# Performance work log

Hardware: AMD Instinct MI355X
Metric: run time of the kernel (lower is better)

The kernel has to match this reference:

```python
import jax, jax.numpy as jnp
import numpy as np

CIN, HID, OUT = 128, 256, 349
NTYPES, ETYPES = 4, 5
N0, N1, N2 = 120000, 40000, 10000
GNODES, GEDGES = 250000, 2000000
E0, E1 = 1500000, 400000


def setup_inputs() -> dict:
    key = jax.random.key(0)
    ks = jax.random.split(key, 24)
    ri = jax.random.randint
    rn = jax.random.normal
    inp = {}
    inp['n_id'] = ri(ks[0], (N0,), 0, GNODES)
    inp['x0'] = rn(ks[1], (100000, CIN), dtype=jnp.float32)
    inp['src0'] = ri(ks[2], (E0,), 0, N0)
    inp['dst0'] = ri(ks[3], (E0,), 0, N1)
    inp['e_id0'] = ri(ks[4], (E0,), 0, GEDGES)
    inp['src1'] = ri(ks[5], (E1,), 0, N1)
    inp['dst1'] = ri(ks[6], (E1,), 0, N2)
    inp['e_id1'] = ri(ks[7], (E1,), 0, GEDGES)
    inp['edge_type'] = ri(ks[8], (GEDGES,), 0, ETYPES)
    inp['node_type'] = ri(ks[9], (GNODES,), 0, NTYPES)
    inp['local_node_idx'] = ri(ks[10], (GNODES,), 0, 50000)
    # learned parameters
    inp['emb1'] = rn(ks[11], (50000, CIN), dtype=jnp.float32)
    inp['emb2'] = rn(ks[12], (50000, CIN), dtype=jnp.float32)
    inp['emb3'] = rn(ks[13], (50000, CIN), dtype=jnp.float32)
    s0 = 1.0 / np.sqrt(CIN)
    s1 = 1.0 / np.sqrt(HID)
    inp['relW0'] = rn(ks[14], (ETYPES, CIN, HID), dtype=jnp.float32) * s0
    inp['rootW0'] = rn(ks[15], (NTYPES, CIN, HID), dtype=jnp.float32) * s0
    inp['rootb0'] = rn(ks[16], (NTYPES, HID), dtype=jnp.float32) * 0.02
    inp['relW1'] = rn(ks[17], (ETYPES, HID, OUT), dtype=jnp.float32) * s1
    inp['rootW1'] = rn(ks[18], (NTYPES, HID, OUT), dtype=jnp.float32) * s1
    inp['rootb1'] = rn(ks[19], (NTYPES, OUT), dtype=jnp.float32) * 0.02
    return inp


def _group_input(tables, node_type, local_node_idx, n_id):
    # RGNN.group_input: per-node-type gather from feature / embedding tables.
    nt = node_type[n_id]            # [N0]
    li = local_node_idx[n_id]       # [N0]
    h = jnp.zeros((n_id.shape[0], CIN), dtype=tables[0].dtype)
    for k, tab in enumerate(tables):
        idx = jnp.minimum(li, tab.shape[0] - 1)
        h = jnp.where((nt == k)[:, None], tab[idx], h)
    return h, nt


def _rgcn_layer(x, nt_src, src, dst, et, relW, rootW, rootb, n_tgt):
    # out = sum_t mean-aggregate(x_j over edges of type t) @ W_t  (linear commutes with mean)
    T = relW.shape[0]
    xj = x[src]                                           # [E, Cin] gather
    seg = dst * T + et                                    # fused (target, edge_type) segment id
    sums = jax.ops.segment_sum(xj, seg, num_segments=n_tgt * T)
    cnts = jax.ops.segment_sum(jnp.ones((src.shape[0],), x.dtype), seg, num_segments=n_tgt * T)
    mean = (sums / jnp.maximum(cnts, 1.0)[:, None]).reshape(n_tgt, T, -1)  # [Nt, T, Cin]
    out = jnp.einsum('ntc,tco->no', mean, relW)           # [Nt, Cout]
    # per-node-type root linear: out[mask] += root_lins[i](x_target[mask])
    x_t = x[:n_tgt]
    nt_t = nt_src[:n_tgt]
    allr = jnp.einsum('nc,tco->tno', x_t, rootW) + rootb[:, None, :]  # [Tn, Nt, Cout]
    root = jnp.take_along_axis(allr, nt_t[None, :, None], axis=0)[0]
    return out + root


def reference(n_id, x0, src0, dst0, e_id0, src1, dst1, e_id1, edge_type, node_type,
              local_node_idx, emb1, emb2, emb3, relW0, rootW0, rootb0, relW1, rootW1, rootb1):
    h, nt = _group_input([x0, emb1, emb2, emb3], node_type, local_node_idx, n_id)
    # layer 0: I -> H
    h = _rgcn_layer(h, nt, src0, dst0, edge_type[e_id0], relW0, rootW0, rootb0, N1)
    h = jax.nn.relu(h)
    nt = nt[:N1]
    # layer 1: H -> O
    h = _rgcn_layer(h, nt, src1, dst1, edge_type[e_id1], relW1, rootW1, rootb1, N2)
    return jax.nn.log_softmax(h, axis=-1)
```

## Files before the change

### kernel.cpp

```cpp
#include <hip/hip_runtime.h>
#include <hip/hip_bf16.h>
#include <cmath>

constexpr int kCIN = 128, kHID = 256, kOUT = 349;
constexpr int kNT = 4, kET = 5;
constexpr int kN0 = 120000, kN1 = 40000, kN2 = 10000;
constexpr int kNSEG0 = kN1 * kET;
constexpr int kNSEG1 = kN2 * kET;
constexpr int kNSEG = kNSEG0 + kNSEG1;

constexpr int kBinSegs = 512;
constexpr int kNBin0 = (kNSEG0 + kBinSegs - 1) / kBinSegs;
constexpr int kNBin1 = (kNSEG1 + kBinSegs - 1) / kBinSegs;
constexpr int kNBin  = kNBin0 + kNBin1;
constexpr int kNBLK  = 512;
constexpr int kSB    = 128;

typedef __bf16 bf16x8 __attribute__((ext_vector_type(8)));
typedef float f32x4 __attribute__((ext_vector_type(4)));
typedef float f32x2v __attribute__((ext_vector_type(2)));
typedef unsigned short ushort8v __attribute__((ext_vector_type(8)));

__device__ __forceinline__ unsigned short f2b(float f) {
    unsigned int b = __float_as_uint(f);
    unsigned int r = (b + 0x7FFFu + ((b >> 16) & 1u)) >> 16;
    return (unsigned short)r;
}
__device__ __forceinline__ float b2f(unsigned short u) {
    return __uint_as_float((unsigned int)u << 16);
}
__device__ __forceinline__ void gl2lds16(const void* g, void* l) {
    __builtin_amdgcn_global_load_lds(
        (const __attribute__((address_space(1))) void*)g,
        (__attribute__((address_space(3))) void*)l, 16, 0, 0);
}

__device__ __forceinline__ unsigned int f2e4m3(float f) {
#if __has_builtin(__builtin_amdgcn_cvt_pk_fp8_f32)
    return (unsigned int)(__builtin_amdgcn_cvt_pk_fp8_f32(f, f, 0, false) & 0xFF);
#else
    unsigned int sb = (__float_as_uint(f) >> 31) << 7;
    float m = fminf(fabsf(f), 448.f);
    unsigned int code;
    if (m < 0.015625f) {
        code = (unsigned int)__float2int_rn(m * 512.f);
    } else {
        unsigned int b = __float_as_uint(m);
        b = b + 0x7FFFF + ((b >> 20) & 1);
        int e8 = (int)(b >> 23) - 120;
        if (e8 > 15) code = 0x7E;
        else code = ((unsigned int)e8 << 3) | ((b >> 20) & 7);
    }
    return sb | code;
#endif
}

__device__ __forceinline__ void e4m3x4_to_f32(unsigned int u, float* o4) {
#if __has_builtin(__builtin_amdgcn_cvt_pk_f32_fp8)
    f32x2v a = __builtin_amdgcn_cvt_pk_f32_fp8(u, false);
    f32x2v b = __builtin_amdgcn_cvt_pk_f32_fp8(u, true);
    o4[0] = a[0]; o4[1] = a[1]; o4[2] = b[0]; o4[3] = b[1];
#else
#pragma unroll
    for (int i = 0; i < 4; i++) {
        unsigned int c = (u >> (8 * i)) & 0xFF;
        unsigned int s = c >> 7, e = (c >> 3) & 15, mm = c & 7;
        float v;
        if (e == 0) v = (float)mm * 0.001953125f;
        else        v = __uint_as_float((e + 120u) << 23 | mm << 20);
        o4[i] = s ? -v : v;
    }
#endif
}

__global__ void k_et8(const int* __restrict__ etype, unsigned char* __restrict__ et8, int n)
{
    int i = blockIdx.x * 256 + threadIdx.x;
    if (i < n) et8[i] = (unsigned char)etype[i];
}

__global__ void k_gather(const int* __restrict__ n_id, const float* __restrict__ x0,
                         const float* __restrict__ e1, const float* __restrict__ e2,
                         const float* __restrict__ e3, const int* __restrict__ ntype,
                         const int* __restrict__ lidx, unsigned short* __restrict__ h0b,
                         unsigned char* __restrict__ h0f8, int* __restrict__ nt0)
{
    int row = blockIdx.x * 8 + (threadIdx.x >> 5);
    if (row >= kN0) return;
    int lane = threadIdx.x & 31;
    int gid = n_id[row];
    int nt = ntype[gid];
    int li = lidx[gid];
    const float* tab;
    int rows;
    if (nt == 0)      { tab = x0; rows = 100000; }
    else if (nt == 1) { tab = e1; rows = 50000; }
    else if (nt == 2) { tab = e2; rows = 50000; }
    else              { tab = e3; rows = 50000; }
    int idx = li < rows ? li : rows - 1;
    float4 v = reinterpret_cast<const float4*>(tab + (size_t)idx * kCIN)[lane];
    ushort4 o;
    o.x = f2b(v.x); o.y = f2b(v.y); o.z = f2b(v.z); o.w = f2b(v.w);
    reinterpret_cast<ushort4*>(h0b + (size_t)row * kCIN)[lane] = o;
    unsigned int q = f2e4m3(v.x) | (f2e4m3(v.y) << 8) | (f2e4m3(v.z) << 16) | (f2e4m3(v.w) << 24);
    reinterpret_cast<unsigned int*>(h0f8 + (size_t)row * kCIN)[lane] = q;
    if (lane == 0) nt0[row] = nt;
}

__global__ __launch_bounds__(1024) void k_bincnt(
    const int* __restrict__ dst0, const int* __restrict__ eid0, int E0,
    const int* __restrict__ dst1, const int* __restrict__ eid1, int E1,
    const unsigned char* __restrict__ et8, int* __restrict__ cnts2d,
    int* __restrict__ seg32,
    const int* __restrict__ nt0, int* __restrict__ ntcnts)
{
    __shared__ int h[kNBin];
    const int tid = threadIdx.x;
    if (blockIdx.x < kNBLK) {
        for (int k = tid; k < kNBin; k += 1024) h[k] = 0;
        __syncthreads();
        int Etot = E0 + E1;
        int chunk = (Etot + kNBLK - 1) / kNBLK;
        int lo = blockIdx.x * chunk;
        int hi = min(lo + chunk, Etot);
        for (int i = lo + tid; i < hi; i += 1024) {
            int c;
            if (i < E0) c = dst0[i] * kET + (int)et8[eid0[i]];
            else { int e = i - E0; c = kNBin0 * kBinSegs + dst1[e] * kET + (int)et8[eid1[e]]; }
            seg32[i] = c;
            atomicAdd(&h[c >> 9], 1);
        }
        __syncthreads();
        for (int k = tid; k < kNBin; k += 1024) cnts2d[(size_t)k * kNBLK + blockIdx.x] = h[k];
    } else {
        int b = blockIdx.x - kNBLK;
        int layer = b >= kSB;
        int blk = b - layer * kSB;
        int M = layer ? kN2 : kN1;
        if (tid < 4) h[tid] = 0;
        __syncthreads();
        int chunk = (M + kSB - 1) / kSB;
        int lo = blk * chunk, hi = min(lo + chunk, M);
        for (int i = lo + tid; i < hi; i += 1024) atomicAdd(&h[nt0[i]], 1);
        __syncthreads();
        if (tid < 4) ntcnts[(layer * 4 + tid) * kSB + blk] = h[tid];
    }
}

__global__ void k_scan1(const int* __restrict__ cnt, int* __restrict__ excl,
                        int* __restrict__ blksum, int n)
{
    __shared__ int sm[1024];
    int i = blockIdx.x * 1024 + threadIdx.x;
    int v = (i < n) ? cnt[i] : 0;
    sm[threadIdx.x] = v;
    __syncthreads();
    for (int off = 1; off < 1024; off <<= 1) {
        int t = (threadIdx.x >= off) ? sm[threadIdx.x - off] : 0;
        __syncthreads();
        sm[threadIdx.x] += t;
        __syncthreads();
    }
    if (i < n) excl[i] = sm[threadIdx.x] - v;
    if (threadIdx.x == 1023) blksum[blockIdx.x] = sm[1023];
}

__global__ __launch_bounds__(1024) void k_scan2(
    int* __restrict__ blksum, int nblk,
    const int* __restrict__ ntcnts, int* __restrict__ ntoffs,
    int* __restrict__ goff0, int* __restrict__ goff1)
{
    __shared__ int sm[1024];
    int tid = threadIdx.x;
    if (blockIdx.x == 0) {
        int v = (tid < nblk) ? blksum[tid] : 0;
        sm[tid] = v;
        __syncthreads();
        for (int off = 1; off < 1024; off <<= 1) {
            int t = (tid >= off) ? sm[tid - off] : 0;
            __syncthreads();
            sm[tid] += t;
            __syncthreads();
        }
        if (tid < nblk) blksum[tid] = sm[tid] - v;
    } else {
        int v = ntcnts[tid];
        sm[tid] = v;
        __syncthreads();
        for (int off = 1; off < 512; off <<= 1) {
            int t = 0;
            if ((tid & 511) >= off) t = sm[tid - off];
            __syncthreads();
            sm[tid] += t;
            __syncthreads();
        }
        int excl = sm[tid] - v;
        ntoffs[tid] = excl;
        if ((tid & 127) == 0) {
            int layer = tid >> 9;
            int t = (tid >> 7) & 3;
            if (layer == 0) goff0[t] = excl; else goff1[t] = excl;
        }
        if (tid == 0) { goff0[4] = kN1; goff1[4] = kN2; }
    }
}

__global__ __launch_bounds__(1024) void k_binplace(
    const int* __restrict__ src0, int E0,
    const int* __restrict__ src1, int E1,
    const int* __restrict__ seg32,
    const int* __restrict__ offs2d, const int* __restrict__ blksum,
    unsigned int* __restrict__ pairs,
    const int* __restrict__ nt0, const int* __restrict__ ntoffs,
    int* __restrict__ perm0, int* __restrict__ perm1)
{
    __shared__ int cur[kNBin];
    const int tid = threadIdx.x;
    if (blockIdx.x < kNBLK) {
        for (int k = tid; k < kNBin; k += 1024) {
            size_t li = (size_t)k * kNBLK + blockIdx.x;
            cur[k] = offs2d[li] + blksum[li >> 10];
        }
        __syncthreads();
        int Etot = E0 + E1;
        int chunk = (Etot + kNBLK - 1) / kNBLK;
        int lo = blockIdx.x * chunk;
        int hi = min(lo + chunk, Etot);
        for (int i = lo + tid; i < hi; i += 1024) {
            int c = seg32[i];
            int s = (i < E0) ? src0[i] : src1[i - E0];
            unsigned int pay = (unsigned int)s | ((unsigned int)(c & (kBinSegs - 1)) << 17);
            int p = atomicAdd(&cur[c >> 9], 1);
            pairs[p] = pay;
        }
    } else {
        int b = blockIdx.x - kNBLK;
        int layer = b >= kSB;
        int blk = b - layer * kSB;
        int M = layer ? kN2 : kN1;
        int* perm = layer ? perm1 : perm0;
        if (tid < 4) cur[tid] = ntoffs[(layer * 4 + tid) * kSB + blk];
        __syncthreads();
        int chunk = (M + kSB - 1) / kSB;
        int lo = blk * chunk, hi = min(lo + chunk, M);
        for (int i = lo + tid; i < hi; i += 1024) {
            int p = atomicAdd(&cur[nt0[i]], 1);
            perm[p] = i;
        }
    }
}

__global__ __launch_bounds__(1024) void k_binscatter(
    const int* __restrict__ offs2d, const int* __restrict__ blksum, int Etot,
    const unsigned int* __restrict__ pairs,
    int* __restrict__ order, int* __restrict__ starts, int* __restrict__ cnt)
{
    __shared__ int h[kBinSegs];
    __shared__ int sc[kBinSegs];
    __shared__ int cur[kBinSegs];
    const int bin = blockIdx.x;
    const int tid = threadIdx.x;
    size_t bi = (size_t)bin * kNBLK;
    const int base = offs2d[bi] + blksum[bi >> 10];
    int end = Etot;
    if (bin + 1 < kNBin) {
        size_t ei = (size_t)(bin + 1) * kNBLK;
        end = offs2d[ei] + blksum[ei >> 10];
    }
    const int c = end - base;
    const unsigned int* pp = pairs + base;

    for (int k = tid; k < kBinSegs; k += 1024) h[k] = 0;
    __syncthreads();
    for (int j = tid; j < c; j += 1024) atomicAdd(&h[pp[j] >> 17], 1);
    __syncthreads();
    if (tid < kBinSegs) sc[tid] = h[tid];
    __syncthreads();
    for (int off = 1; off < kBinSegs; off <<= 1) {
        int t = 0;
        if (tid < kBinSegs && tid >= off) t = sc[tid - off];
        __syncthreads();
        if (tid < kBinSegs) sc[tid] += t;
        __syncthreads();
    }
    int seg_rel, abs_base, seglim;
    if (bin < kNBin0) { seg_rel = bin * kBinSegs; abs_base = seg_rel; seglim = kNSEG0 - seg_rel; }
    else { seg_rel = (bin - kNBin0) * kBinSegs; abs_base = kNSEG0 + seg_rel; seglim = kNSEG1 - seg_rel; }
    if (tid < kBinSegs) {
        int excl = sc[tid] - h[tid];
        cur[tid] = excl;
        if (tid < seglim) {
            starts[abs_base + tid] = base + excl;
            cnt[abs_base + tid] = h[tid];
        }
    }
    __syncthreads();
    for (int j = tid; j < c; j += 1024) {
        unsigned int u = pp[j];
        int sl = (int)(u >> 17);
        int p = atomicAdd(&cur[sl], 1);
        order[base + p] = (int)(u & 0x1FFFFu);
    }
}

__global__ __launch_bounds__(256) void k_segreduce8(
    const int* __restrict__ starts, const int* __restrict__ cnt,
    const int* __restrict__ order, const unsigned char* __restrict__ h8,
    unsigned short* __restrict__ mean, int nseg)
{
    constexpr int C = kCIN;
    constexpr int L = C / 8;
    constexpr int SPB = 256 / L;
    int sidx = blockIdx.x * SPB + threadIdx.x / L;
    if (sidx >= nseg) return;
    int lane = threadIdx.x % L;
    int st = starts[sidx];
    int n = cnt[sidx];
    const unsigned char* hp = h8 + (size_t)lane * 8;
    float a[4][8];
#pragma unroll
    for (int u = 0; u < 4; u++)
#pragma unroll
        for (int i = 0; i < 8; i++) a[u][i] = 0.f;
    int j = 0;
    for (; j + 4 <= n; j += 4) {
        int s0 = order[st + j + 0];
        int s1 = order[st + j + 1];
        int s2 = order[st + j + 2];
        int s3 = order[st + j + 3];
        uint2 u0 = *reinterpret_cast<const uint2*>(hp + (size_t)s0 * C);
        uint2 u1 = *reinterpret_cast<const uint2*>(hp + (size_t)s1 * C);
        uint2 u2 = *reinterpret_cast<const uint2*>(hp + (size_t)s2 * C);
        uint2 u3 = *reinterpret_cast<const uint2*>(hp + (size_t)s3 * C);
        float d[8];
        e4m3x4_to_f32(u0.x, d); e4m3x4_to_f32(u0.y, d + 4);
#pragma unroll
        for (int i = 0; i < 8; i++) a[0][i] += d[i];
        e4m3x4_to_f32(u1.x, d); e4m3x4_to_f32(u1.y, d + 4);
#pragma unroll
        for (int i = 0; i < 8; i++) a[1][i] += d[i];
        e4m3x4_to_f32(u2.x, d); e4m3x4_to_f32(u2.y, d + 4);
#pragma unroll
        for (int i = 0; i < 8; i++) a[2][i] += d[i];
        e4m3x4_to_f32(u3.x, d); e4m3x4_to_f32(u3.y, d + 4);
#pragma unroll
        for (int i = 0; i < 8; i++) a[3][i] += d[i];
    }
    for (; j < n; ++j) {
        int s0 = order[st + j];
        uint2 u0 = *reinterpret_cast<const uint2*>(hp + (size_t)s0 * C);
        float d[8];
        e4m3x4_to_f32(u0.x, d); e4m3x4_to_f32(u0.y, d + 4);
#pragma unroll
        for (int i = 0; i < 8; i++) a[0][i] += d[i];
    }
    float sc = 1.0f / fmaxf((float)n, 1.0f);
    ushort8v o;
#pragma unroll
    for (int i = 0; i < 8; i++) o[i] = f2b(((a[0][i] + a[1][i]) + (a[2][i] + a[3][i])) * sc);
    *reinterpret_cast<ushort8v*>(mean + (size_t)sidx * C + lane * 8) = o;
}

template<int C>
__global__ __launch_bounds__(256) void k_segreduce(
    const int* __restrict__ starts, const int* __restrict__ cnt,
    const int* __restrict__ order, const unsigned short* __restrict__ h,
    unsigned short* __restrict__ mean, int nseg)
{
    constexpr int L = C / 8;
    constexpr int SPB = 256 / L;
    int sidx = blockIdx.x * SPB + threadIdx.x / L;
    if (sidx >= nseg) return;
    int lane = threadIdx.x % L;
    int st = starts[sidx];
    int n = cnt[sidx];
    const unsigned short* hp = h + (size_t)lane * 8;
    float a[4][8];
#pragma unroll
    for (int u = 0; u < 4; u++)
#pragma unroll
        for (int i = 0; i < 8; i++) a[u][i] = 0.f;
    int j = 0;
    for (; j + 4 <= n; j += 4) {
        int s0 = order[st + j + 0];
        int s1 = order[st + j + 1];
        int s2 = order[st + j + 2];
        int s3 = order[st + j + 3];
        ushort8v v0 = *reinterpret_cast<const ushort8v*>(hp + (size_t)s0 * C);
        ushort8v v1 = *reinterpret_cast<const ushort8v*>(hp + (size_t)s1 * C);
        ushort8v v2 = *reinterpret_cast<const ushort8v*>(hp + (size_t)s2 * C);
        ushort8v v3 = *reinterpret_cast<const ushort8v*>(hp + (size_t)s3 * C);
#pragma unroll
        for (int i = 0; i < 8; i++) {
            a[0][i] += b2f(v0[i]); a[1][i] += b2f(v1[i]);
            a[2][i] += b2f(v2[i]); a[3][i] += b2f(v3[i]);
        }
    }
    for (; j < n; ++j) {
        int s0 = order[st + j];
        ushort8v v0 = *reinterpret_cast<const ushort8v*>(hp + (size_t)s0 * C);
#pragma unroll
        for (int i = 0; i < 8; i++) a[0][i] += b2f(v0[i]);
    }
    float sc = 1.0f / fmaxf((float)n, 1.0f);
    ushort8v o;
#pragma unroll
    for (int i = 0; i < 8; i++) o[i] = f2b(((a[0][i] + a[1][i]) + (a[2][i] + a[3][i])) * sc);
    *reinterpret_cast<ushort8v*>(mean + (size_t)sidx * C + lane * 8) = o;
}

__global__ void k_prepw2(const float* __restrict__ relW0, const float* __restrict__ rootW0,
                         unsigned short* __restrict__ Bt0T,
                         const float* __restrict__ relW1, const float* __restrict__ rootW1,
                         unsigned short* __restrict__ Bt1T)
{
    constexpr int T0 = kNT * 256 * 768;
    constexpr int T1 = kNT * 384 * 1536;
    int i = blockIdx.x * 256 + threadIdx.x;
    if (i < T0) {
        int g = i / (256 * 768);
        int rem = i - g * (256 * 768);
        int col = rem / 768;
        int k = rem - col * 768;
        float v = (k < 640) ? relW0[(size_t)k * 256 + col]
                            : rootW0[((size_t)g * 128 + (k - 640)) * 256 + col];
        Bt0T[i] = f2b(v);
    } else if (i < T0 + T1) {
        int ii = i - T0;
        int g = ii / (384 * 1536);
        int rem = ii - g * (384 * 1536);
        int col = rem / 1536;
        int k = rem - col * 1536;
        float v = 0.f;
        if (col < kOUT) v = (k < 1280) ? relW1[(size_t)k * kOUT + col]
                                       : rootW1[((size_t)g * 256 + (k - 1280)) * kOUT + col];
        Bt1T[ii] = f2b(v);
    }
}

template<int C, int BM, int BN, int RELU, int OUTBF16>
__global__ __launch_bounds__(256) void k_gemm_sorted(
    int M, int Nreal, int NpadK,
    const unsigned short* __restrict__ meanb,
    const unsigned short* __restrict__ hb,
    const unsigned short* __restrict__ BtT,
    const float* __restrict__ rootb,
    const int* __restrict__ perm, const int* __restrict__ goff,
    unsigned short* __restrict__ outb, float* __restrict__ outf)
{
    constexpr int K1 = kET * C;
    constexpr int K  = K1 + C;
    constexpr int FM = BM / 32;
    constexpr int FN = BN / 32;
    __shared__ __align__(16) char ldsA[BM * 128];
    __shared__ __align__(16) char ldsB[BN * 128];

    int g, row0s = 0, gend = 0;
    {
        int gs0 = goff[0], gs1 = goff[1], gs2 = goff[2], gs3 = goff[3], gs4 = goff[4];
        int gs[5] = {gs0, gs1, gs2, gs3, gs4};
        int t = blockIdx.x, tb = 0;
        for (g = 0; g < 4; ++g) {
            int cg = gs[g + 1] - gs[g];
            int ntl = (cg + BM - 1) / BM;
            if (t < tb + ntl) { row0s = gs[g] + (t - tb) * BM; gend = gs[g + 1]; break; }
            tb += ntl;
        }
        if (g == 4) return;
    }
    const int rows_here = min(BM, gend - row0s);
    const unsigned short* BtG = BtT + (size_t)g * NpadK;

    const int tid = threadIdx.x;
    const int col0 = blockIdx.y * BN;
    const int wid = tid >> 6, lane = tid & 63;
    const int wrow = (wid >> 1) * (BM / 2);
    const int wcol = (wid & 1) * (BN / 2);
    const int lr = lane >> 3;
    const int kb = (lane & 7) * 16;

    f32x4 acc[FM][FN] = {};

    for (int k0 = 0; k0 < K; k0 += 64) {
        const bool inMean = (k0 < K1);
        const size_t kB = (size_t)k0 * 2;
#pragma unroll
        for (int c2 = 0; c2 < BM / 32; ++c2) {
            int rb = (wid * (BM / 32) + c2) * 8;
            int r = rb + lr;
            int pr = perm[row0s + min(r, rows_here - 1)];
            const char* rowp = inMean
                ? (const char*)(meanb + (size_t)pr * K1) + kB
                : (const char*)(hb + (size_t)pr * C) + (kB - (size_t)K1 * 2);
            gl2lds16(rowp + (kb ^ ((r & 7) << 4)), &ldsA[rb * 128]);
        }
#pragma unroll
        for (int c2 = 0; c2 < BN / 32; ++c2) {
            int rb = (wid * (BN / 32) + c2) * 8;
            int r = rb + lr;
            const char* rowp = (const char*)(BtG + (size_t)(col0 + r) * K) + kB;
            gl2lds16(rowp + (kb ^ ((r & 7) << 4)), &ldsB[rb * 128]);
        }
        __syncthreads();
#pragma unroll
        for (int kc = 0; kc < 2; kc++) {
            int kb2 = kc * 64 + (lane >> 4) * 16;
            bf16x8 af[FM], bfr[FN];
#pragma unroll
            for (int m = 0; m < FM; m++) {
                int r = wrow + m * 16 + (lane & 15);
                af[m] = *reinterpret_cast<const bf16x8*>(&ldsA[r * 128 + (kb2 ^ ((r & 7) << 4))]);
            }
#pragma unroll
            for (int n = 0; n < FN; n++) {
                int r = wcol + n * 16 + (lane & 15);
                bfr[n] = *reinterpret_cast<const bf16x8*>(&ldsB[r * 128 + (kb2 ^ ((r & 7) << 4))]);
            }
#pragma unroll
            for (int m = 0; m < FM; m++)
#pragma unroll
                for (int n = 0; n < FN; n++)
                    acc[m][n] = __builtin_amdgcn_mfma_f32_16x16x32_bf16(af[m], bfr[n], acc[m][n], 0, 0, 0);
        }
        __syncthreads();
    }

#pragma unroll
    for (int m = 0; m < FM; m++) {
        int rlb = wrow + m * 16 + (lane >> 4) * 4;
#pragma unroll
        for (int n = 0; n < FN; n++) {
            int col = col0 + wcol + n * 16 + (lane & 15);
            if (col >= Nreal) continue;
            f32x4 v = acc[m][n];
#pragma unroll
            for (int j = 0; j < 4; j++) {
                int rl = rlb + j;
                if (rl >= rows_here) continue;
                int orig = perm[row0s + rl];
                float x = v[j] + rootb[g * Nreal + col];
                if (RELU) x = fmaxf(x, 0.f);
                if (OUTBF16) outb[(size_t)orig * Nreal + col] = f2b(x);
                else         outf[(size_t)orig * Nreal + col] = x;
            }
        }
    }
}

__global__ void k_logsm(float* __restrict__ out, int M, int N)
{
    int row = blockIdx.x * 4 + (threadIdx.x >> 6);
    if (row >= M) return;
    int lane = threadIdx.x & 63;
    float* p = out + (size_t)row * N;
    float mx = -3.4e38f;
    for (int c = lane; c < N; c += 64) mx = fmaxf(mx, p[c]);
#pragma unroll
    for (int o = 32; o > 0; o >>= 1) mx = fmaxf(mx, __shfl_xor(mx, o));
    float s = 0.f;
    for (int c = lane; c < N; c += 64) s += expf(p[c] - mx);
#pragma unroll
    for (int o = 32; o > 0; o >>= 1) s += __shfl_xor(s, o);
    float lse = mx + logf(s);
    for (int c = lane; c < N; c += 64) p[c] -= lse;
}

extern "C" void kernel_launch(void* const* d_in, const int* in_sizes, int n_in,
                              void* d_out, int out_size, void* d_ws, size_t ws_size,
                              hipStream_t stream)
{
    const int*   n_id   = (const int*)d_in[0];
    const float* x0     = (const float*)d_in[1];
    const int*   src0   = (const int*)d_in[2];
    const int*   dst0   = (const int*)d_in[3];
    const int*   eid0   = (const int*)d_in[4];
    const int*   src1   = (const int*)d_in[5];
    const int*   dst1   = (const int*)d_in[6];
    const int*   eid1   = (const int*)d_in[7];
    const int*   etype  = (const int*)d_in[8];
    const int*   ntype  = (const int*)d_in[9];
    const int*   lidx   = (const int*)d_in[10];
    const float* emb1   = (const float*)d_in[11];
    const float* emb2   = (const float*)d_in[12];
    const float* emb3   = (const float*)d_in[13];
    const float* relW0  = (const float*)d_in[14];
    const float* rootW0 = (const float*)d_in[15];
    const float* rootb0 = (const float*)d_in[16];
    const float* relW1  = (const float*)d_in[17];
    const float* rootW1 = (const float*)d_in[18];
    const float* rootb1 = (const float*)d_in[19];
    float* out = (float*)d_out;

    const int E0 = in_sizes[2];
    const int E1 = in_sizes[5];
    const int Etot = E0 + E1;
    const int nET = in_sizes[8];
    constexpr int K0s  = kET * kCIN + kCIN;
    constexpr int K1s  = kET * kHID + kHID;
    constexpr int Npad0 = 256;
    constexpr int Npad1 = 384;

    char* ws = (char*)d_ws;
    size_t off = 0;
    auto alloc = [&](size_t bytes) -> void* {
        void* p = ws + off;
        off = (off + bytes + 255) & ~(size_t)255;
        return p;
    };
    unsigned short* h0b   = (unsigned short*)alloc((size_t)kN0 * kCIN * 2);
    unsigned char*  h0f8  = (unsigned char*)alloc((size_t)kN0 * kCIN);
    int*            nt0   = (int*)alloc((size_t)kN0 * 4);
    unsigned short* meanb = (unsigned short*)alloc((size_t)kNSEG0 * kCIN * 2);
    int*            cnt    = (int*)alloc((size_t)kNSEG * 4);
    int*            starts = (int*)alloc((size_t)kNSEG * 4);
    int*            cnts2d = (int*)alloc((size_t)kNBin * kNBLK * 4);
    int*            offs2d = (int*)alloc((size_t)kNBin * kNBLK * 4);
    int*            blksum = (int*)alloc(1024 * 4);
    unsigned int*   pairs  = (unsigned int*)alloc((size_t)Etot * 4);
    int*            order  = (int*)alloc((size_t)Etot * 4);
    int*            seg32  = (int*)alloc((size_t)Etot * 4);
    unsigned char*  et8    = (unsigned char*)alloc((size_t)nET);
    unsigned short* h1b   = (unsigned short*)alloc((size_t)kN1 * kHID * 2);
    unsigned short* Bt0T  = (unsigned short*)alloc((size_t)kNT * Npad0 * K0s * 2);
    unsigned short* Bt1T  = (unsigned short*)alloc((size_t)kNT * Npad1 * K1s * 2);
    int*            perm0  = (int*)alloc((size_t)kN1 * 4);
    int*            goff0  = (int*)alloc(8 * 4);
    int*            perm1  = (int*)alloc((size_t)kN2 * 4);
    int*            goff1  = (int*)alloc(8 * 4);
    int*            ntcnts = (int*)alloc(1024 * 4);
    int*            ntoffs = (int*)alloc(1024 * 4);

    constexpr int TPREP = kNT * Npad0 * K0s + kNT * Npad1 * K1s;
    k_prepw2<<<(TPREP + 255) / 256, 256, 0, stream>>>(relW0, rootW0, Bt0T, relW1, rootW1, Bt1T);
    k_et8<<<(nET + 255) / 256, 256, 0, stream>>>(etype, et8, nET);
    k_gather<<<(kN0 + 7) / 8, 256, 0, stream>>>(n_id, x0, emb1, emb2, emb3, ntype, lidx, h0b, h0f8, nt0);

    k_bincnt<<<kNBLK + 2 * kSB, 1024, 0, stream>>>(dst0, eid0, E0, dst1, eid1, E1, et8,
                                                   cnts2d, seg32, nt0, ntcnts);
    int nscan = kNBin * kNBLK;
    int nblk = (nscan + 1023) / 1024;
    k_scan1<<<nblk, 1024, 0, stream>>>(cnts2d, offs2d, blksum, nscan);
    k_scan2<<<2, 1024, 0, stream>>>(blksum, nblk, ntcnts, ntoffs, goff0, goff1);
    k_binplace<<<kNBLK + 2 * kSB, 1024, 0, stream>>>(src0, E0, src1, E1, seg32,
                                                     offs2d, blksum, pairs, nt0, ntoffs, perm0, perm1);
    k_binscatter<<<kNBin, 1024, 0, stream>>>(offs2d, blksum, Etot, pairs, order, starts, cnt);

    k_segreduce8<<<(kNSEG0 + 15) / 16, 256, 0, stream>>>(starts, cnt, order, h0f8, meanb, kNSEG0);
    dim3 g0(kN1 / 64 + 4, Npad0 / 128);
    k_gemm_sorted<kCIN, 64, 128, 1, 1><<<g0, 256, 0, stream>>>(
        kN1, kHID, Npad0 * K0s, meanb, h0b, Bt0T, rootb0, perm0, goff0, h1b, nullptr);

    k_segreduce<kHID><<<(kNSEG1 + 7) / 8, 256, 0, stream>>>(starts + kNSEG0, cnt + kNSEG0, order, h1b, meanb, kNSEG1);
    dim3 g1(kN2 / 64 + 5, Npad1 / 128);
    k_gemm_sorted<kHID, 64, 128, 0, 0><<<g1, 256, 0, stream>>>(
        kN2, kOUT, Npad1 * K1s, meanb, h1b, Bt1T, rootb1, perm1, goff1, nullptr, out);

    k_logsm<<<(kN2 + 3) / 4, 256, 0, stream>>>(out, kN2, kOUT);
}
```

Baseline: 251.4 us.

## Use fp8 hidden features for layer-1 aggregation, widen segreduce loads, merge prep kernels

The layer-0 GEMM epilogue now also writes an e4m3 copy of the hidden activations. Layer-1 mean aggregation reads that fp8 copy instead of bf16, which halves the gather traffic. The segment-reduce kernel is templated, uses 16-byte loads per lane with two accumulators, and replaces the bf16 reduction kernel. The weight-prep and edge-type conversion kernels are merged into one launch. The cost is an extra fp8 store in the GEMM epilogue and lower precision in the layer-1 mean.

```diff
diff --git a/kernel.cpp b/kernel.cpp
--- a/kernel.cpp
+++ b/kernel.cpp
@@ -73,10 +73,38 @@
 #endif
 }
 
-__global__ void k_et8(const int* __restrict__ etype, unsigned char* __restrict__ et8, int n)
-{
+__global__ void k_prep(const float* __restrict__ relW0, const float* __restrict__ rootW0,
+                       unsigned short* __restrict__ Bt0T,
+                       const float* __restrict__ relW1, const float* __restrict__ rootW1,
+                       unsigned short* __restrict__ Bt1T,
+                       const int* __restrict__ etype, unsigned char* __restrict__ et8, int nET)
+{
+    constexpr int T0 = kNT * 256 * 768;
+    constexpr int T1 = kNT * 384 * 1536;
+    constexpr int TP = T0 + T1;
     int i = blockIdx.x * 256 + threadIdx.x;
-    if (i < n) et8[i] = (unsigned char)etype[i];
+    if (i < T0) {
+        int g = i / (256 * 768);
+        int rem = i - g * (256 * 768);
+        int col = rem / 768;
+        int k = rem - col * 768;
+        float v = (k < 640) ? relW0[(size_t)k * 256 + col]
+                            : rootW0[((size_t)g * 128 + (k - 640)) * 256 + col];
+        Bt0T[i] = f2b(v);
+    } else if (i < TP) {
+        int ii = i - T0;
+        int g = ii / (384 * 1536);
+        int rem = ii - g * (384 * 1536);
+        int col = rem / 1536;
+        int k = rem - col * 1536;
+        float v = 0.f;
+        if (col < kOUT) v = (k < 1280) ? relW1[(size_t)k * kOUT + col]
+                                       : rootW1[((size_t)g * 256 + (k - 1280)) * kOUT + col];
+        Bt1T[ii] = f2b(v);
+    } else {
+        int k = i - TP;
+        if (k < nET) et8[k] = (unsigned char)etype[k];
+    }
 }
 
 __global__ void k_gather(const int* __restrict__ n_id, const float* __restrict__ x0,
@@ -303,142 +331,61 @@
     }
 }
 
+template<int C>
 __global__ __launch_bounds__(256) void k_segreduce8(
     const int* __restrict__ starts, const int* __restrict__ cnt,
     const int* __restrict__ order, const unsigned char* __restrict__ h8,
     unsigned short* __restrict__ mean, int nseg)
 {
-    constexpr int C = kCIN;
-    constexpr int L = C / 8;
+    constexpr int L = C / 16;
     constexpr int SPB = 256 / L;
     int sidx = blockIdx.x * SPB + threadIdx.x / L;
     if (sidx >= nseg) return;
     int lane = threadIdx.x % L;
     int st = starts[sidx];
     int n = cnt[sidx];
-    const unsigned char* hp = h8 + (size_t)lane * 8;
-    float a[4][8];
-#pragma unroll
-    for (int u = 0; u < 4; u++)
-#pragma unroll
-        for (int i = 0; i < 8; i++) a[u][i] = 0.f;
+    const unsigned char* hp = h8 + (size_t)lane * 16;
+    float a0[16], a1[16];
+#pragma unroll
+    for (int i = 0; i < 16; i++) { a0[i] = 0.f; a1[i] = 0.f; }
     int j = 0;
-    for (; j + 4 <= n; j += 4) {
+    for (; j + 2 <= n; j += 2) {
         int s0 = order[st + j + 0];
         int s1 = order[st + j + 1];
-        int s2 = order[st + j + 2];
-        int s3 = order[st + j + 3];
-        uint2 u0 = *reinterpret_cast<const uint2*>(hp + (size_t)s0 * C);
-        uint2 u1 = *reinterpret_cast<const uint2*>(hp + (size_t)s1 * C);
-        uint2 u2 = *reinterpret_cast<const uint2*>(hp + (size_t)s2 * C);
-        uint2 u3 = *reinterpret_cast<const uint2*>(hp + (size_t)s3 * C);
-        float d[8];
+        uint4 u0 = *reinterpret_cast<const uint4*>(hp + (size_t)s0 * C);
+        uint4 u1 = *reinterpret_cast<const uint4*>(hp + (size_t)s1 * C);
+        float d[16];
         e4m3x4_to_f32(u0.x, d); e4m3x4_to_f32(u0.y, d + 4);
-#pragma unroll
-        for (int i = 0; i < 8; i++) a[0][i] += d[i];
+        e4m3x4_to_f32(u0.z, d + 8); e4m3x4_to_f32(u0.w, d + 12);
+#pragma unroll
+        for (int i = 0; i < 16; i++) a0[i] += d[i];
         e4m3x4_to_f32(u1.x, d); e4m3x4_to_f32(u1.y, d + 4);
-#pragma unroll
-        for (int i = 0; i < 8; i++) a[1][i] += d[i];
-        e4m3x4_to_f32(u2.x, d); e4m3x4_to_f32(u2.y, d + 4);
-#pragma unroll
-        for (int i = 0; i < 8; i++) a[2][i] += d[i];
-        e4m3x4_to_f32(u3.x, d); e4m3x4_to_f32(u3.y, d + 4);
-#pragma unroll
-        for (int i = 0; i < 8; i++) a[3][i] += d[i];
-    }
-    for (; j < n; ++j) {
+        e4m3x4_to_f32(u1.z, d + 8); e4m3x4_to_f32(u1.w, d + 12);
+#pragma unroll
+        for (int i = 0; i < 16; i++) a1[i] += d[i];
+    }
+    if (j < n) {
         int s0 = order[st + j];
-        uint2 u0 = *reinterpret_cast<const uint2*>(hp + (size_t)s0 * C);
-        float d[8];
+        uint4 u0 = *reinterpret_cast<const uint4*>(hp + (size_t)s0 * C);
+        float d[16];
         e4m3x4_to_f32(u0.x, d); e4m3x4_to_f32(u0.y, d + 4);
-#pragma unroll
-        for (int i = 0; i < 8; i++) a[0][i] += d[i];
+        e4m3x4_to_f32(u0.z, d + 8); e4m3x4_to_f32(u0.w, d + 12);
+#pragma unroll
+        for (int i = 0; i < 16; i++) a0[i] += d[i];
     }
     float sc = 1.0f / fmaxf((float)n, 1.0f);
-    ushort8v o;
-#pragma unroll
-    for (int i = 0; i < 8; i++) o[i] = f2b(((a[0][i] + a[1][i]) + (a[2][i] + a[3][i])) * sc);
-    *reinterpret_cast<ushort8v*>(mean + (size_t)sidx * C + lane * 8) = o;
-}
-
-template<int C>
-__global__ __launch_bounds__(256) void k_segreduce(
-    const int* __restrict__ starts, const int* __restrict__ cnt,
-    const int* __restrict__ order, const unsigned short* __restrict__ h,
-    unsigned short* __restrict__ mean, int nseg)
-{
-    constexpr int L = C / 8;
-    constexpr int SPB = 256 / L;
-    int sidx = blockIdx.x * SPB + threadIdx.x / L;
-    if (sidx >= nseg) return;
-    int lane = threadIdx.x % L;
-    int st = starts[sidx];
-    int n = cnt[sidx];
-    const unsigned short* hp = h + (size_t)lane * 8;
-    float a[4][8];
-#pragma unroll
-    for (int u = 0; u < 4; u++)
-#pragma unroll
-        for (int i = 0; i < 8; i++) a[u][i] = 0.f;
-    int j = 0;
-    for (; j + 4 <= n; j += 4) {
-        int s0 = order[st + j + 0];
-        int s1 = order[st + j + 1];
-        int s2 = order[st + j + 2];
-        int s3 = order[st + j + 3];
-        ushort8v v0 = *reinterpret_cast<const ushort8v*>(hp + (size_t)s0 * C);
-        ushort8v v1 = *reinterpret_cast<const ushort8v*>(hp + (size_t)s1 * C);
-        ushort8v v2 = *reinterpret_cast<const ushort8v*>(hp + (size_t)s2 * C);
-        ushort8v v3 = *reinterpret_cast<const ushort8v*>(hp + (size_t)s3 * C);
-#pragma unroll
-        for (int i = 0; i < 8; i++) {
-            a[0][i] += b2f(v0[i]); a[1][i] += b2f(v1[i]);
-            a[2][i] += b2f(v2[i]); a[3][i] += b2f(v3[i]);
-        }
-    }
-    for (; j < n; ++j) {
-        int s0 = order[st + j];
-        ushort8v v0 = *reinterpret_cast<const ushort8v*>(hp + (size_t)s0 * C);
-#pragma unroll
-        for (int i = 0; i < 8; i++) a[0][i] += b2f(v0[i]);
-    }
-    float sc = 1.0f / fmaxf((float)n, 1.0f);
-    ushort8v o;
-#pragma unroll
-    for (int i = 0; i < 8; i++) o[i] = f2b(((a[0][i] + a[1][i]) + (a[2][i] + a[3][i])) * sc);
-    *reinterpret_cast<ushort8v*>(mean + (size_t)sidx * C + lane * 8) = o;
-}
-
-__global__ void k_prepw2(const float* __restrict__ relW0, const float* __restrict__ rootW0,
-                         unsigned short* __restrict__ Bt0T,
-                         const float* __restrict__ relW1, const float* __restrict__ rootW1,
-                         unsigned short* __restrict__ Bt1T)
-{
-    constexpr int T0 = kNT * 256 * 768;
-    constexpr int T1 = kNT * 384 * 1536;
-    int i = blockIdx.x * 256 + threadIdx.x;
-    if (i < T0) {
-        int g = i / (256 * 768);
-        int rem = i - g * (256 * 768);
-        int col = rem / 768;
-        int k = rem - col * 768;
-        float v = (k < 640) ? relW0[(size_t)k * 256 + col]
-                            : rootW0[((size_t)g * 128 + (k - 640)) * 256 + col];
-        Bt0T[i] = f2b(v);
-    } else if (i < T0 + T1) {
-        int ii = i - T0;
-        int g = ii / (384 * 1536);
-        int rem = ii - g * (384 * 1536);
-        int col = rem / 1536;
-        int k = rem - col * 1536;
-        float v = 0.f;
-        if (col < kOUT) v = (k < 1280) ? relW1[(size_t)k * kOUT + col]
-                                       : rootW1[((size_t)g * 256 + (k - 1280)) * kOUT + col];
-        Bt1T[ii] = f2b(v);
-    }
-}
-
-template<int C, int BM, int BN, int RELU, int OUTBF16>
+    ushort8v o0, o1;
+#pragma unroll
+    for (int i = 0; i < 8; i++) {
+        o0[i] = f2b((a0[i] + a1[i]) * sc);
+        o1[i] = f2b((a0[i + 8] + a1[i + 8]) * sc);
+    }
+    unsigned short* mp = mean + (size_t)sidx * C + lane * 16;
+    *reinterpret_cast<ushort8v*>(mp) = o0;
+    *reinterpret_cast<ushort8v*>(mp + 8) = o1;
+}
+
+template<int C, int BM, int BN, int RELU, int OUTBF16, int OUTF8>
 __global__ __launch_bounds__(256) void k_gemm_sorted(
     int M, int Nreal, int NpadK,
     const unsigned short* __restrict__ meanb,
@@ -446,7 +393,8 @@
     const unsigned short* __restrict__ BtT,
     const float* __restrict__ rootb,
     const int* __restrict__ perm, const int* __restrict__ goff,
-    unsigned short* __restrict__ outb, float* __restrict__ outf)
+    unsigned short* __restrict__ outb, float* __restrict__ outf,
+    unsigned char* __restrict__ outf8)
 {
     constexpr int K1 = kET * C;
     constexpr int K  = K1 + C;
@@ -540,8 +488,12 @@
                 int orig = perm[row0s + rl];
                 float x = v[j] + rootb[g * Nreal + col];
                 if (RELU) x = fmaxf(x, 0.f);
-                if (OUTBF16) outb[(size_t)orig * Nreal + col] = f2b(x);
-                else         outf[(size_t)orig * Nreal + col] = x;
+                if (OUTBF16) {
+                    outb[(size_t)orig * Nreal + col] = f2b(x);
+                    if (OUTF8) outf8[(size_t)orig * Nreal + col] = (unsigned char)f2e4m3(x);
+                } else {
+                    outf[(size_t)orig * Nreal + col] = x;
+                }
             }
         }
     }
@@ -621,6 +573,7 @@
     int*            seg32  = (int*)alloc((size_t)Etot * 4);
     unsigned char*  et8    = (unsigned char*)alloc((size_t)nET);
     unsigned short* h1b   = (unsigned short*)alloc((size_t)kN1 * kHID * 2);
+    unsigned char*  h1f8  = (unsigned char*)alloc((size_t)kN1 * kHID);
     unsigned short* Bt0T  = (unsigned short*)alloc((size_t)kNT * Npad0 * K0s * 2);
     unsigned short* Bt1T  = (unsigned short*)alloc((size_t)kNT * Npad1 * K1s * 2);
     int*            perm0  = (int*)alloc((size_t)kN1 * 4);
@@ -631,8 +584,9 @@
     int*            ntoffs = (int*)alloc(1024 * 4);
 
     constexpr int TPREP = kNT * Npad0 * K0s + kNT * Npad1 * K1s;
-    k_prepw2<<<(TPREP + 255) / 256, 256, 0, stream>>>(relW0, rootW0, Bt0T, relW1, rootW1, Bt1T);
-    k_et8<<<(nET + 255) / 256, 256, 0, stream>>>(etype, et8, nET);
+    int prep_total = TPREP + nET;
+    k_prep<<<(prep_total + 255) / 256, 256, 0, stream>>>(relW0, rootW0, Bt0T, relW1, rootW1, Bt1T,
+                                                         etype, et8, nET);
     k_gather<<<(kN0 + 7) / 8, 256, 0, stream>>>(n_id, x0, emb1, emb2, emb3, ntype, lidx, h0b, h0f8, nt0);
 
     k_bincnt<<<kNBLK + 2 * kSB, 1024, 0, stream>>>(dst0, eid0, E0, dst1, eid1, E1, et8,
@@ -645,15 +599,15 @@
                                                      offs2d, blksum, pairs, nt0, ntoffs, perm0, perm1);
     k_binscatter<<<kNBin, 1024, 0, stream>>>(offs2d, blksum, Etot, pairs, order, starts, cnt);
 
-    k_segreduce8<<<(kNSEG0 + 15) / 16, 256, 0, stream>>>(starts, cnt, order, h0f8, meanb, kNSEG0);
+    k_segreduce8<kCIN><<<(kNSEG0 + 31) / 32, 256, 0, stream>>>(starts, cnt, order, h0f8, meanb, kNSEG0);
     dim3 g0(kN1 / 64 + 4, Npad0 / 128);
-    k_gemm_sorted<kCIN, 64, 128, 1, 1><<<g0, 256, 0, stream>>>(
-        kN1, kHID, Npad0 * K0s, meanb, h0b, Bt0T, rootb0, perm0, goff0, h1b, nullptr);
-
-    k_segreduce<kHID><<<(kNSEG1 + 7) / 8, 256, 0, stream>>>(starts + kNSEG0, cnt + kNSEG0, order, h1b, meanb, kNSEG1);
+    k_gemm_sorted<kCIN, 64, 128, 1, 1, 1><<<g0, 256, 0, stream>>>(
+        kN1, kHID, Npad0 * K0s, meanb, h0b, Bt0T, rootb0, perm0, goff0, h1b, nullptr, h1f8);
+
+    k_segreduce8<kHID><<<(kNSEG1 + 15) / 16, 256, 0, stream>>>(starts + kNSEG0, cnt + kNSEG0, order, h1f8, meanb, kNSEG1);
     dim3 g1(kN2 / 64 + 5, Npad1 / 128);
-    k_gemm_sorted<kHID, 64, 128, 0, 0><<<g1, 256, 0, stream>>>(
-        kN2, kOUT, Npad1 * K1s, meanb, h1b, Bt1T, rootb1, perm1, goff1, nullptr, out);
+    k_gemm_sorted<kHID, 64, 128, 0, 0, 0><<<g1, 256, 0, stream>>>(
+        kN2, kOUT, Npad1 * K1s, meanb, h1b, Bt1T, rootb1, perm1, goff1, nullptr, out, nullptr);
 
     k_logsm<<<(kN2 + 3) / 4, 256, 0, stream>>>(out, kN2, kOUT);
 }
```

Measured after the change: 244.5 us. -2.8%, faster.
